# Performance work log

Measured on AMD Instinct MI355X. Metric: run time of the kernel, lower is better.

The kernel has to match this reference:

```python
import jax, jax.numpy as jnp
import numpy as np

B, L = 8, 512
EMB, NHEAD, HD = 512, 8, 64
FFN, NL = 2048, 6
VOCAB, NRE, RING_START, PAD, MAXLEN = 45, 20, 24, 0, 512
NOUT0 = VOCAB - NRE  # 25
NEG = -jnp.inf


def _ln(x, g, b, eps=1e-5):
    m = jnp.mean(x, -1, keepdims=True)
    v = jnp.mean((x - m) ** 2, -1, keepdims=True)
    return (x - m) * jax.lax.rsqrt(v + eps) * g + b


def setup_inputs():
    key = jax.random.key(0)
    ks = jax.random.split(key, 24)
    p = lambda k, shape: jax.random.normal(k, shape, jnp.float32) * 0.02
    return {
        "sequences": jax.random.randint(ks[0], (B, L), 1, VOCAB),  # avoid PAD=0
        "count_sequences": jax.random.randint(ks[1], (B, L), 0, MAXLEN),
        "graph_mask_sequences": jax.random.bernoulli(ks[2], 0.05, (B, L, VOCAB)),
        "valence_mask_sequences": jax.random.bernoulli(ks[3], 0.05, (B, L, VOCAB)),
        "linear_loc_squares": jax.random.randint(ks[4], (B, L, L), 0, MAXLEN + 1),
        "up_loc_squares": jax.random.randint(ks[5], (B, L, L), 0, MAXLEN + 1),
        "down_loc_squares": jax.random.randint(ks[6], (B, L, L), 0, MAXLEN + 1),
        "tok_emb": p(ks[7], (VOCAB, EMB)),
        "cnt_emb": p(ks[8], (MAXLEN, EMB)),
        "lin_loc_emb": p(ks[9], (MAXLEN + 1, NHEAD)),
        "up_loc_emb": p(ks[10], (MAXLEN + 1, NHEAD)),
        "down_loc_emb": p(ks[11], (MAXLEN + 1, NHEAD)),
        "in_proj_w": p(ks[12], (NL, 3 * EMB, EMB)),
        "in_proj_b": jnp.zeros((NL, 3 * EMB), jnp.float32),
        "out_w": p(ks[13], (NL, EMB, EMB)),
        "out_b": jnp.zeros((NL, EMB), jnp.float32),
        "ln1_g": jnp.ones((NL, EMB), jnp.float32),
        "ln1_b": jnp.zeros((NL, EMB), jnp.float32),
        "ln2_g": jnp.ones((NL, EMB), jnp.float32),
        "ln2_b": jnp.zeros((NL, EMB), jnp.float32),
        "ffn_w1": p(ks[14], (NL, FFN, EMB)),
        "ffn_b1": jnp.zeros((NL, FFN), jnp.float32),
        "ffn_w2": p(ks[15], (NL, EMB, FFN)),
        "ffn_b2": jnp.zeros((NL, EMB), jnp.float32),
        "fin_g": jnp.ones((EMB,), jnp.float32),
        "fin_b": jnp.zeros((EMB,), jnp.float32),
        "gen_w": p(ks[16], (NOUT0, EMB)),
        "gen_b": jnp.zeros((NOUT0,), jnp.float32),
        "ring_w0": p(ks[17], (EMB, EMB)),
        "ring_b0": jnp.zeros((EMB,), jnp.float32),
        "ring_w1": p(ks[18], (EMB, EMB)),
        "ring_b1": jnp.zeros((EMB,), jnp.float32),
    }


def _forward(tok_emb, cnt_emb, lin_loc_emb, up_loc_emb, down_loc_emb,
             in_proj_w, in_proj_b, out_w, out_b, ln1_g, ln1_b, ln2_g, ln2_b,
             ffn_w1, ffn_b1, ffn_w2, ffn_b2, fin_g, fin_b, gen_w, gen_b,
             ring_w0, ring_b0, ring_w1, ring_b1,
             sequences, count_sequences, graph_mask_sequences,
             valence_mask_sequences, linear_loc_squares, up_loc_squares,
             down_loc_squares):
    scale_e = jnp.sqrt(jnp.float32(EMB))
    x = tok_emb[sequences] * scale_e + cnt_emb[count_sequences] * scale_e  # (B,L,E)

    # per-head additive attention bias from three (B,L,L) index lookups
    bias = lin_loc_emb[linear_loc_squares] + up_loc_emb[up_loc_squares] + down_loc_emb[down_loc_squares]  # (B,L,L,H)
    bias = jnp.transpose(bias, (0, 3, 1, 2))  # (B,H,Lq,Lk)
    causal = jnp.tril(jnp.ones((L, L), bool))
    attn_bias = jnp.where(causal[None, None], bias, NEG)
    pad = sequences == PAD  # key padding
    attn_bias = jnp.where(pad[:, None, None, :], NEG, attn_bias)

    inv_sqrt_hd = 1.0 / jnp.sqrt(jnp.float32(HD))
    for i in range(NL):  # post-norm TransformerEncoderLayer, gelu
        qkv = jnp.einsum('ble,fe->blf', x, in_proj_w[i]) + in_proj_b[i]
        q, k, v = jnp.split(qkv, 3, axis=-1)
        q = q.reshape(B, L, NHEAD, HD)
        k = k.reshape(B, L, NHEAD, HD)
        v = v.reshape(B, L, NHEAD, HD)
        scores = jnp.einsum('bqhd,bkhd->bhqk', q, k) * inv_sqrt_hd + attn_bias
        a = jax.nn.softmax(scores, axis=-1)
        ctx = jnp.einsum('bhqk,bkhd->bqhd', a, v).reshape(B, L, EMB)
        attn_out = jnp.einsum('ble,fe->blf', ctx, out_w[i]) + out_b[i]
        x = _ln(x + attn_out, ln1_g[i], ln1_b[i])
        h = jax.nn.gelu(jnp.einsum('ble,fe->blf', x, ffn_w1[i]) + ffn_b1[i], approximate=False)
        ff = jnp.einsum('blf,ef->ble', h, ffn_w2[i]) + ffn_b2[i]
        x = _ln(x + ff, ln2_g[i], ln2_b[i])
    x = _ln(x, fin_g, fin_b)

    logits0 = jnp.einsum('ble,oe->blo', x, gen_w) + gen_b  # (B,L,NOUT0)

    # EdgeLogitLayer: scatter ring-start projections into NRE slots
    out0 = jnp.einsum('ble,he->blh', x, ring_w0) + ring_b0
    out1_ = jnp.einsum('ble,he->blh', x, ring_w1) + ring_b1
    ring_start = sequences == RING_START
    idx = jnp.where(ring_start, jnp.cumsum(ring_start.astype(jnp.int32), axis=1), 0)  # (B,L)
    bidx = jnp.arange(B)[:, None]
    slots = jnp.zeros((B, NRE + 1, EMB), x.dtype).at[bidx, idx].set(out1_, mode='drop')
    ring_tab = slots[:, 1:]  # drop slot 0 (non-ring-start writes)
    logits1 = jnp.einsum('ble,bre->blr', out0, ring_tab) * (EMB ** -0.5)

    logits = jnp.concatenate([logits0, logits1], axis=2)  # (B,L,VOCAB)
    logits = jnp.where(graph_mask_sequences, NEG, logits)
    logits = jnp.where(valence_mask_sequences, NEG, logits)
    return logits


def reference(sequences, count_sequences, graph_mask_sequences, valence_mask_sequences,
              linear_loc_squares, up_loc_squares, down_loc_squares,
              tok_emb, cnt_emb, lin_loc_emb, up_loc_emb, down_loc_emb,
              in_proj_w, in_proj_b, out_w, out_b, ln1_g, ln1_b, ln2_g, ln2_b,
              ffn_w1, ffn_b1, ffn_w2, ffn_b2, fin_g, fin_b, gen_w, gen_b,
              ring_w0, ring_b0, ring_w1, ring_b1):
    return _forward(tok_emb, cnt_emb, lin_loc_emb, up_loc_emb, down_loc_emb,
                    in_proj_w, in_proj_b, out_w, out_b, ln1_g, ln1_b, ln2_g, ln2_b,
                    ffn_w1, ffn_b1, ffn_w2, ffn_b2, fin_g, fin_b, gen_w, gen_b,
                    ring_w0, ring_b0, ring_w1, ring_b1,
                    sequences, count_sequences, graph_mask_sequences,
                    valence_mask_sequences, linear_loc_squares, up_loc_squares,
                    down_loc_squares)
```

## Files before the change

### kernel.cpp

```cpp
#include <hip/hip_runtime.h>
#include <cmath>

#define BB 8
#define LL 512
#define EMB 512
#define NHEAD 8
#define HD 64
#define FFN 2048
#define NL 6
#define VOCAB 45
#define NRE 20
#define RING_START 24
#define NOUT0 25
#define BL 4096

#define BIG_NEG -1.0e30f

typedef __bf16 bf16x8 __attribute__((ext_vector_type(8)));
typedef __bf16 bf16x4 __attribute__((ext_vector_type(4)));
typedef float f32x4 __attribute__((ext_vector_type(4)));

__device__ __forceinline__ void ld_g2l(const __bf16* g, __bf16* l) {
  __builtin_amdgcn_global_load_lds(
      (const __attribute__((address_space(1))) unsigned int*)g,
      (__attribute__((address_space(3))) unsigned int*)l, 16, 0, 0);
}

__device__ __forceinline__ int xcd_swizzle_lin() {
  const int nwg = gridDim.x * gridDim.y * gridDim.z;
  int lin = blockIdx.x + gridDim.x * (blockIdx.y + gridDim.y * blockIdx.z);
  if ((nwg & 7) == 0) lin = (lin & 7) * (nwg >> 3) + (lin >> 3);
  return lin;
}

__device__ __forceinline__ float gelu_fast(float v) {
  const float u = v * 0.70710678118654752f;
  const float a = fabsf(u);
  const float t = 1.0f / fmaf(0.3275911f, a, 1.0f);
  float p = fmaf(1.061405429f, t, -1.453152027f);
  p = fmaf(p, t, 1.421413741f);
  p = fmaf(p, t, -0.284496736f);
  p = fmaf(p, t, 0.254829592f);
  p *= t;
  const float er = 1.0f - p * __expf(-a * a);
  const float ers = (u < 0.f) ? -er : er;
  return 0.5f * v * (1.0f + ers);
}

__global__ __launch_bounds__(256) void megacast_kernel(
    const float* __restrict__ s0, const float* __restrict__ s1,
    const float* __restrict__ s2, const float* __restrict__ s3,
    const float* __restrict__ s4, const float* __restrict__ s5,
    const float* __restrict__ s6, const float* __restrict__ s7,
    const float* __restrict__ s8, __bf16* __restrict__ dw,
    __bf16* __restrict__ dt) {
  const int gid = blockIdx.x * 256 + threadIdx.x;
  const int szs[9] = {589824, 196608, 786432, 786432, 32768,
                      32768,  513,    513,    513};
  const float* srcs[9] = {s0, s1, s2, s3, s4, s5, s6, s7, s8};
  int seg = 0, base = 0;
  while (seg < 9 && gid >= base + szs[seg]) { base += szs[seg]; seg++; }
  if (seg >= 9) return;
  const int local = gid - base;
  const float* src = srcs[seg];
  const float4 a = ((const float4*)src)[local * 2];
  const float4 b = ((const float4*)src)[local * 2 + 1];
  bf16x8 v;
  v[0] = (__bf16)a.x; v[1] = (__bf16)a.y; v[2] = (__bf16)a.z; v[3] = (__bf16)a.w;
  v[4] = (__bf16)b.x; v[5] = (__bf16)b.y; v[6] = (__bf16)b.z; v[7] = (__bf16)b.w;
  __bf16* dst = (seg < 6) ? (dw + (size_t)base * 8 + (size_t)local * 8)
                          : (dt + (size_t)(seg - 6) * 4104 + (size_t)local * 8);
  *(bf16x8*)dst = v;
}

__global__ __launch_bounds__(128) void embed_kernel(
    const int* __restrict__ seq, const int* __restrict__ cnt,
    const float* __restrict__ tok_emb, const float* __restrict__ cnt_emb,
    float* __restrict__ x, __bf16* __restrict__ xb) {
  const int row = blockIdx.x;
  const int t = seq[row];
  const int c = cnt[row];
  const float scale = 22.627416997969522f;
  const int j = threadIdx.x * 4;
  float4 tv = *(const float4*)(tok_emb + (size_t)t * EMB + j);
  float4 cv = *(const float4*)(cnt_emb + (size_t)c * EMB + j);
  float4 o;
  o.x = (tv.x + cv.x) * scale;
  o.y = (tv.y + cv.y) * scale;
  o.z = (tv.z + cv.z) * scale;
  o.w = (tv.w + cv.w) * scale;
  *(float4*)(x + (size_t)row * EMB + j) = o;
  bf16x4 h;
  h[0] = (__bf16)o.x; h[1] = (__bf16)o.y; h[2] = (__bf16)o.z; h[3] = (__bf16)o.w;
  *(bf16x4*)(xb + (size_t)row * EMB + j) = h;
}

__global__ __launch_bounds__(256) void bias_kernel(
    const int* __restrict__ lin_sq, const int* __restrict__ up_sq,
    const int* __restrict__ down_sq,
    const __bf16* __restrict__ tl16, const __bf16* __restrict__ tu16,
    const __bf16* __restrict__ td16,
    const int* __restrict__ seq, __bf16* __restrict__ bias) {
  __shared__ __bf16 Tl[513 * 8], Tu[513 * 8], Td[513 * 8];
  __shared__ int seqs[LL];
  const int tid = threadIdx.x;
  const int b = blockIdx.x >> 6;
  const int q0 = (blockIdx.x & 63) * 8;
  for (int i = tid; i < 513; i += 256) {
    *(bf16x8*)&Tl[i * 8] = *(const bf16x8*)&tl16[i * 8];
    *(bf16x8*)&Tu[i * 8] = *(const bf16x8*)&tu16[i * 8];
    *(bf16x8*)&Td[i * 8] = *(const bf16x8*)&td16[i * 8];
  }
  for (int i = tid; i < LL; i += 256) seqs[i] = seq[b * LL + i];
  __syncthreads();
  for (int q = q0; q < q0 + 8; q++) {
    const size_t rbase = ((size_t)(b * LL + q)) * LL;
    for (int k = tid; k <= q; k += 256) {
      const int li = lin_sq[rbase + k], ui = up_sq[rbase + k],
                di = down_sq[rbase + k];
      const bool valid = (seqs[k] != 0);
      bf16x8 a = *(const bf16x8*)&Tl[li * 8];
      bf16x8 u = *(const bf16x8*)&Tu[ui * 8];
      bf16x8 d = *(const bf16x8*)&Td[di * 8];
#pragma unroll
      for (int h = 0; h < NHEAD; h++) {
        float v = valid ? ((float)a[h] + (float)u[h] + (float)d[h])
                        : -INFINITY;
        bias[(((size_t)(b * NHEAD + h) * LL) + q) * LL + k] = (__bf16)v;
      }
    }
  }
}

template <int BM, int BN, int ACT, int OUTBF, int RES, int B2, int SPLITK>
__global__ __launch_bounds__(256) void gemm_mfma_kernel(
    const __bf16* __restrict__ A, const __bf16* __restrict__ W,
    const float* __restrict__ bias, const float* __restrict__ bias2,
    float* __restrict__ C, __bf16* __restrict__ Cb,
    const float* __restrict__ Res, int N, int K, int lda) {
  constexpr int MI = BM / 32;
  constexpr int NI = BN / 32;
  constexpr int LV = (BM == 128 ? 4 : 2) + (BN == 128 ? 4 : 2);
  __shared__ __bf16 As[2][BM * 64];
  __shared__ __bf16 Ws[2][BN * 64];
  const int tid = threadIdx.x;
  const int lane = tid & 63, wave = tid >> 6;
  const int wm = wave >> 1, wn = wave & 1;
  const int q = lane >> 4, l15 = lane & 15;

  const int lin = xcd_swizzle_lin();
  const int bx = lin % gridDim.x;
  const int by = (lin / gridDim.x) % gridDim.y;
  const int kz = SPLITK ? (lin / (gridDim.x * gridDim.y)) : 0;
  const int m0 = by * BM, n0 = bx * BN;

  const int sr = tid >> 3;
  const int sc = (tid & 7) ^ (sr & 7);
  const __bf16* Ag = A + (size_t)(m0 + sr) * lda + sc * 8 + (size_t)kz * K;
  const __bf16* Wg = W + (size_t)(n0 + sr) * lda + sc * 8 + (size_t)kz * K;

  auto stage = [&](int buf, int k0) {
    __bf16* Al = &As[buf][tid * 8];
    __bf16* Wl = &Ws[buf][tid * 8];
    ld_g2l(Ag + k0, Al);
    ld_g2l(Ag + k0 + (size_t)32 * lda, Al + 2048);
    if constexpr (BM == 128) {
      ld_g2l(Ag + k0 + (size_t)64 * lda, Al + 4096);
      ld_g2l(Ag + k0 + (size_t)96 * lda, Al + 6144);
    }
    ld_g2l(Wg + k0, Wl);
    ld_g2l(Wg + k0 + (size_t)32 * lda, Wl + 2048);
    if constexpr (BN == 128) {
      ld_g2l(Wg + k0 + (size_t)64 * lda, Wl + 4096);
      ld_g2l(Wg + k0 + (size_t)96 * lda, Wl + 6144);
    }
  };

  f32x4 acc[MI][NI] = {};

  stage(0, 0);
  int cur = 0;
  for (int k0 = 0; k0 < K; k0 += 64) {
    if (k0 + 64 < K) {
      stage(cur ^ 1, k0 + 64);
      if constexpr (LV == 4)
        asm volatile("s_waitcnt vmcnt(4)" ::: "memory");
      else if constexpr (LV == 6)
        asm volatile("s_waitcnt vmcnt(6)" ::: "memory");
      else
        asm volatile("s_waitcnt vmcnt(8)" ::: "memory");
    } else {
      asm volatile("s_waitcnt vmcnt(0)" ::: "memory");
    }
    __builtin_amdgcn_s_barrier();
    __builtin_amdgcn_sched_barrier(0);
#pragma unroll
    for (int kh = 0; kh < 2; kh++) {
      bf16x8 af[MI], bfr[NI];
      const int ch = ((kh * 4 + q) ^ (l15 & 7)) * 8;
#pragma unroll
      for (int mi = 0; mi < MI; mi++)
        af[mi] = *(const bf16x8*)&As[cur]
                     [(wm * (BM / 2) + mi * 16 + l15) * 64 + ch];
#pragma unroll
      for (int ni = 0; ni < NI; ni++)
        bfr[ni] = *(const bf16x8*)&Ws[cur]
                      [(wn * (BN / 2) + ni * 16 + l15) * 64 + ch];
#pragma unroll
      for (int mi = 0; mi < MI; mi++)
#pragma unroll
        for (int ni = 0; ni < NI; ni++)
          acc[mi][ni] = __builtin_amdgcn_mfma_f32_16x16x32_bf16(
              af[mi], bfr[ni], acc[mi][ni], 0, 0, 0);
    }
    __builtin_amdgcn_sched_barrier(0);
    __builtin_amdgcn_s_barrier();
    cur ^= 1;
  }

  float* Cz = SPLITK ? (C + (size_t)kz * ((size_t)BL * N)) : C;
#pragma unroll
  for (int ni = 0; ni < NI; ni++) {
    const int n = n0 + wn * (BN / 2) + ni * 16 + l15;
    float bv = 0.f;
    if (!SPLITK || kz == 0)
      bv = (B2 && n >= EMB) ? bias2[n - EMB] : bias[n];
#pragma unroll
    for (int mi = 0; mi < MI; mi++) {
#pragma unroll
      for (int r = 0; r < 4; r++) {
        const int m = m0 + wm * (BM / 2) + mi * 16 + q * 4 + r;
        float v = acc[mi][ni][r] + bv;
        if (RES && (!SPLITK || kz == 0)) v += Res[(size_t)m * N + n];
        if (ACT == 1) v = gelu_fast(v);
        if (OUTBF)
          Cb[(size_t)m * N + n] = (__bf16)v;
        else
          Cz[(size_t)m * N + n] = v;
      }
    }
  }
}

__global__ __launch_bounds__(256) void attn_tile2_kernel(
    const __bf16* __restrict__ qkv, const __bf16* __restrict__ bias,
    __bf16* __restrict__ Po, float2* __restrict__ Pml,
    __bf16* __restrict__ ctx) {
  __shared__ __bf16 Ks[64][72];
  __shared__ __bf16 Vt[64][72];
  __shared__ __bf16 Ps[64][72];
  const int tid = threadIdx.x;
  const int lane = tid & 63, w = tid >> 6;
  const int q = lane >> 4, l15 = lane & 15;
  const int lin = xcd_swizzle_lin();
  const int pidx = lin % gridDim.x;
  const int bh = lin / gridDim.x;
  const int b = bh >> 3, h = bh & 7;
  int qt = 0, acc0 = 0;
  while (acc0 + (qt / 2 + 1) <= pidx) { acc0 += qt / 2 + 1; qt++; }
  const int j = pidx - acc0;
  const int q0 = qt * 64;
  const int slot = (bh * 8 + qt) * 4 + j;
  const bool direct = (qt <= 1);
  const float inv_sqrt_hd = 0.125f;

  const int srow = tid >> 2, c0 = (tid & 3) * 16;
  {
    const __bf16* qsrc =
        qkv + (size_t)(b * LL + q0 + srow) * 1536 + h * HD + c0;
    *(bf16x8*)&Ps[srow][c0] = *(const bf16x8*)qsrc;
    *(bf16x8*)&Ps[srow][c0 + 8] = *(const bf16x8*)(qsrc + 8);
  }
  __syncthreads();
  const bf16x8 aq0 = *(const bf16x8*)&Ps[w * 16 + l15][q * 8];
  const bf16x8 aq1 = *(const bf16x8*)&Ps[w * 16 + l15][32 + q * 8];

  f32x4 o4[4] = {};
  float m[4], l[4];
#pragma unroll
  for (int r = 0; r < 4; r++) { m[r] = -INFINITY; l[r] = 0.f; }

  const int ktEnd = (2 * j + 1 <= qt) ? (2 * j + 1) : qt;
  for (int kt = 2 * j; kt <= ktEnd; kt++) {
    const int k0 = kt * 64;
    __syncthreads();
    {
      const __bf16* src = qkv + (size_t)(b * LL + k0 + srow) * 1536 + h * HD;
      bf16x8 kv0 = *(const bf16x8*)(src + 512 + c0);
      bf16x8 kv1 = *(const bf16x8*)(src + 512 + c0 + 8);
      bf16x8 vv0 = *(const bf16x8*)(src + 1024 + c0);
      bf16x8 vv1 = *(const bf16x8*)(src + 1024 + c0 + 8);
      const __bf16* bsrc =
          bias + ((size_t)bh * LL + (q0 + srow)) * LL + k0 + c0;
      bf16x8 bb0 = *(const bf16x8*)bsrc;
      bf16x8 bb1 = *(const bf16x8*)(bsrc + 8);
      *(bf16x8*)&Ks[srow][c0] = kv0;
      *(bf16x8*)&Ks[srow][c0 + 8] = kv1;
      *(bf16x8*)&Ps[srow][c0] = bb0;
      *(bf16x8*)&Ps[srow][c0 + 8] = bb1;
#pragma unroll
      for (int jj = 0; jj < 8; jj++) {
        Vt[c0 + jj][srow] = vv0[jj];
        Vt[c0 + 8 + jj][srow] = vv1[jj];
      }
    }
    __syncthreads();

    f32x4 s4[4] = {};
    __builtin_amdgcn_s_setprio(1);
#pragma unroll
    for (int ni = 0; ni < 4; ni++) {
      bf16x8 bk0 = *(const bf16x8*)&Ks[ni * 16 + l15][q * 8];
      bf16x8 bk1 = *(const bf16x8*)&Ks[ni * 16 + l15][32 + q * 8];
      s4[ni] =
          __builtin_amdgcn_mfma_f32_16x16x32_bf16(aq0, bk0, s4[ni], 0, 0, 0);
      s4[ni] =
          __builtin_amdgcn_mfma_f32_16x16x32_bf16(aq1, bk1, s4[ni], 0, 0, 0);
    }
    __builtin_amdgcn_s_setprio(0);

    const bool diag = (kt == qt);
#pragma unroll
    for (int r = 0; r < 4; r++) {
      const int qrow = w * 16 + q * 4 + r;
      float sv[4];
#pragma unroll
      for (int ni = 0; ni < 4; ni++) {
        sv[ni] = s4[ni][r] * inv_sqrt_hd +
                 (float)Ps[qrow][ni * 16 + l15];
        if (diag && (ni * 16 + l15 > qrow)) sv[ni] = -INFINITY;
      }
      float tm = fmaxf(fmaxf(sv[0], sv[1]), fmaxf(sv[2], sv[3]));
#pragma unroll
      for (int off = 1; off < 16; off <<= 1)
        tm = fmaxf(tm, __shfl_xor(tm, off, 16));
      const float mnew = fmaxf(m[r], tm);
      const float alpha = expf(m[r] - mnew);
      float rs = 0.f;
#pragma unroll
      for (int ni = 0; ni < 4; ni++) {
        const float p = expf(sv[ni] - mnew);
        Ps[qrow][ni * 16 + l15] = (__bf16)p;
        rs += p;
      }
#pragma unroll
      for (int off = 1; off < 16; off <<= 1) rs += __shfl_xor(rs, off, 16);
      l[r] = l[r] * alpha + rs;
      m[r] = mnew;
#pragma unroll
      for (int ni = 0; ni < 4; ni++) o4[ni][r] *= alpha;
    }
    __syncthreads();

    {
      bf16x8 ap0 = *(const bf16x8*)&Ps[w * 16 + l15][q * 8];
      bf16x8 ap1 = *(const bf16x8*)&Ps[w * 16 + l15][32 + q * 8];
      __builtin_amdgcn_s_setprio(1);
#pragma unroll
      for (int ni = 0; ni < 4; ni++) {
        bf16x8 bv0 = *(const bf16x8*)&Vt[ni * 16 + l15][q * 8];
        bf16x8 bv1 = *(const bf16x8*)&Vt[ni * 16 + l15][32 + q * 8];
        o4[ni] =
            __builtin_amdgcn_mfma_f32_16x16x32_bf16(ap0, bv0, o4[ni], 0, 0, 0);
        o4[ni] =
            __builtin_amdgcn_mfma_f32_16x16x32_bf16(ap1, bv1, o4[ni], 0, 0, 0);
      }
      __builtin_amdgcn_s_setprio(0);
    }
  }

  if (direct) {
#pragma unroll
    for (int r = 0; r < 4; r++) {
      const int qrow = w * 16 + q * 4 + r;
      const float inv = 1.0f / l[r];
      __bf16* dst = ctx + (size_t)(b * LL + q0 + qrow) * EMB + h * HD + l15;
#pragma unroll
      for (int ni = 0; ni < 4; ni++) dst[ni * 16] = (__bf16)(o4[ni][r] * inv);
    }
  } else {
#pragma unroll
    for (int r = 0; r < 4; r++) {
      const int qrow = w * 16 + q * 4 + r;
      if (l15 == 0)
        Pml[(size_t)slot * 64 + qrow] = make_float2(m[r], l[r]);
      __bf16* dst = Po + (size_t)slot * 4096 + qrow * 64 + l15;
#pragma unroll
      for (int ni = 0; ni < 4; ni++) dst[ni * 16] = (__bf16)o4[ni][r];
    }
  }
}

__global__ __launch_bounds__(256) void attn_combine_kernel(
    const __bf16* __restrict__ Po, const float2* __restrict__ Pml,
    __bf16* __restrict__ ctx) {
  const int tid = threadIdx.x;
  const int bh = blockIdx.x / 6;
  const int qt = (blockIdx.x % 6) + 2;
  const int b = bh >> 3, h = bh & 7;
  const int nsl = qt / 2 + 1;
  const int slot0 = (bh * 8 + qt) * 4;
  __shared__ float wls[4][64];
  __shared__ float invl[64];
  if (tid < 64) {
    float mg = -3.0e38f;
    for (int s = 0; s < nsl; s++)
      mg = fmaxf(mg, Pml[(size_t)(slot0 + s) * 64 + tid].x);
    float lsum = 0.f;
    for (int s = 0; s < nsl; s++) {
      const float2 ml = Pml[(size_t)(slot0 + s) * 64 + tid];
      const float wk = expf(ml.x - mg);
      wls[s][tid] = wk;
      lsum += ml.y * wk;
    }
    invl[tid] = 1.0f / lsum;
  }
  __syncthreads();
  const int row = tid >> 2, d0 = (tid & 3) * 16;
  float acc[16] = {};
  for (int s = 0; s < nsl; s++) {
    const __bf16* src = Po + (size_t)(slot0 + s) * 4096 + row * 64 + d0;
    const float wk = wls[s][row];
    bf16x8 v0 = *(const bf16x8*)src;
    bf16x8 v1 = *(const bf16x8*)(src + 8);
#pragma unroll
    for (int jj = 0; jj < 8; jj++) {
      acc[jj] += (float)v0[jj] * wk;
      acc[8 + jj] += (float)v1[jj] * wk;
    }
  }
  const float il = invl[row];
  bf16x8 o0, o1;
#pragma unroll
  for (int jj = 0; jj < 8; jj++) {
    o0[jj] = (__bf16)(acc[jj] * il);
    o1[jj] = (__bf16)(acc[8 + jj] * il);
  }
  __bf16* dst = ctx + (size_t)(b * LL + qt * 64 + row) * EMB + h * HD + d0;
  *(bf16x8*)dst = o0;
  *(bf16x8*)(dst + 8) = o1;
}

template <int NSUM>
__global__ __launch_bounds__(256) void add_ln_kernel(
    const float* __restrict__ xin, const float* __restrict__ g,
    const float* __restrict__ bta, float* __restrict__ out,
    __bf16* __restrict__ outb) {
  const int row = blockIdx.x;
  const int tid = threadIdx.x;
  float v0 = 0.f, v1 = 0.f;
#pragma unroll
  for (int sId = 0; sId < NSUM; sId++) {
    const float* xr = xin + (size_t)sId * BL * EMB + (size_t)row * EMB;
    v0 += xr[tid * 2];
    v1 += xr[tid * 2 + 1];
  }
  float s = v0 + v1, ss = v0 * v0 + v1 * v1;
#pragma unroll
  for (int off = 1; off < 64; off <<= 1) {
    s += __shfl_xor(s, off, 64);
    ss += __shfl_xor(ss, off, 64);
  }
  __shared__ float sbuf[8];
  const int wave = tid >> 6, lane = tid & 63;
  if (lane == 0) { sbuf[wave] = s; sbuf[4 + wave] = ss; }
  __syncthreads();
  s = sbuf[0] + sbuf[1] + sbuf[2] + sbuf[3];
  ss = sbuf[4] + sbuf[5] + sbuf[6] + sbuf[7];
  const float mean = s * (1.0f / EMB);
  const float var = ss * (1.0f / EMB) - mean * mean;
  const float rstd = rsqrtf(var + 1e-5f);
  const float o0 = (v0 - mean) * rstd * g[tid * 2] + bta[tid * 2];
  const float o1 = (v1 - mean) * rstd * g[tid * 2 + 1] + bta[tid * 2 + 1];
  float* orow = out + (size_t)row * EMB;
  orow[tid * 2] = o0;
  orow[tid * 2 + 1] = o1;
  if (outb) {
    __bf16* brow = outb + (size_t)row * EMB;
    brow[tid * 2] = (__bf16)o0;
    brow[tid * 2 + 1] = (__bf16)o1;
  }
}

__global__ __launch_bounds__(512) void ring_scatter_kernel(
    const int* __restrict__ seq, const float* __restrict__ o01,
    float* __restrict__ ring_tab) {
  const int b = blockIdx.x;
  const int tid = threadIdx.x;
  float* rt = ring_tab + (size_t)b * NRE * EMB;
  __shared__ int pos[NRE];
  __shared__ int wcnt[8];
  __shared__ int total;
  const bool flag = (seq[b * LL + tid] == RING_START);
  const unsigned long long msk = __ballot(flag);
  const int wave = tid >> 6, lane = tid & 63;
  if (lane == 0) wcnt[wave] = __popcll(msk);
  for (int i = tid; i < NRE * EMB; i += 512) rt[i] = 0.f;
  __syncthreads();
  if (flag) {
    int base = 0;
    for (int w2 = 0; w2 < wave; w2++) base += wcnt[w2];
    const int ord = base + __popcll(msk & ((1ull << lane) - 1ull));
    if (ord < NRE) pos[ord] = tid;
  }
  if (tid == 0) {
    int t = 0;
    for (int w2 = 0; w2 < 8; w2++) t += wcnt[w2];
    total = (t < NRE) ? t : NRE;
  }
  __syncthreads();
  const int n = total;
  for (int r = 0; r < n; r++) {
    const float* src = o01 + (size_t)(b * LL + pos[r]) * 1024 + 512;
    rt[r * EMB + tid] = src[tid];
  }
}

__global__ __launch_bounds__(256) void head_kernel(
    const float* __restrict__ xf, const float* __restrict__ o01,
    const float* __restrict__ ring_tab, const float* __restrict__ gen_w,
    const float* __restrict__ gen_b, const int* __restrict__ gmask,
    const int* __restrict__ vmask, float* __restrict__ out) {
  const int row = blockIdx.x;
  const int b = row >> 9;
  const int tid = threadIdx.x;
  __shared__ float xr[EMB], o0s[EMB];
  {
    float2 a = ((const float2*)(xf + (size_t)row * EMB))[tid];
    ((float2*)xr)[tid] = a;
    float2 c = ((const float2*)(o01 + (size_t)row * 1024))[tid];
    ((float2*)o0s)[tid] = c;
  }
  __syncthreads();
  const int wave = tid >> 6, lane = tid & 63;
  for (int o = wave; o < VOCAB; o += 4) {
    const float* wrow;
    const float* src;
    float bv, scale;
    if (o < NOUT0) {
      wrow = gen_w + (size_t)o * EMB;
      bv = gen_b[o];
      src = xr;
      scale = 1.0f;
    } else {
      wrow = ring_tab + ((size_t)b * NRE + (o - NOUT0)) * EMB;
      bv = 0.0f;
      src = o0s;
      scale = 0.044194173824159216f;
    }
    float sum = 0.f;
#pragma unroll
    for (int j = 0; j < 8; j++) {
      const int d = lane + 64 * j;
      sum += src[d] * wrow[d];
    }
#pragma unroll
    for (int off = 1; off < 64; off <<= 1) sum += __shfl_xor(sum, off, 64);
    if (lane == 0) {
      float v = sum * scale + bv;
      const size_t oidx = (size_t)row * VOCAB + o;
      if (gmask[oidx] != 0 || vmask[oidx] != 0) v = BIG_NEG;
      out[oidx] = v;
    }
  }
}

extern "C" void kernel_launch(void* const* d_in, const int* in_sizes, int n_in,
                              void* d_out, int out_size, void* d_ws,
                              size_t ws_size, hipStream_t stream) {
  const int* seq = (const int*)d_in[0];
  const int* cnt = (const int*)d_in[1];
  const int* gmask = (const int*)d_in[2];
  const int* vmask = (const int*)d_in[3];
  const int* lin_sq = (const int*)d_in[4];
  const int* up_sq = (const int*)d_in[5];
  const int* down_sq = (const int*)d_in[6];
  const float* tok_emb = (const float*)d_in[7];
  const float* cnt_emb = (const float*)d_in[8];
  const float* lin_e = (const float*)d_in[9];
  const float* up_e = (const float*)d_in[10];
  const float* down_e = (const float*)d_in[11];
  const float* in_proj_w = (const float*)d_in[12];
  const float* in_proj_b = (const float*)d_in[13];
  const float* out_w = (const float*)d_in[14];
  const float* out_b = (const float*)d_in[15];
  const float* ln1_g = (const float*)d_in[16];
  const float* ln1_b = (const float*)d_in[17];
  const float* ln2_g = (const float*)d_in[18];
  const float* ln2_b = (const float*)d_in[19];
  const float* ffn_w1 = (const float*)d_in[20];
  const float* ffn_b1 = (const float*)d_in[21];
  const float* ffn_w2 = (const float*)d_in[22];
  const float* ffn_b2 = (const float*)d_in[23];
  const float* fin_g = (const float*)d_in[24];
  const float* fin_b = (const float*)d_in[25];
  const float* gen_w = (const float*)d_in[26];
  const float* gen_b = (const float*)d_in[27];
  const float* ring_w0 = (const float*)d_in[28];
  const float* ring_b0 = (const float*)d_in[29];
  const float* ring_w1 = (const float*)d_in[30];
  const float* ring_b1 = (const float*)d_in[31];

  char* p = (char*)d_ws;
  auto alloc_f = [&](size_t n) { float* r = (float*)p; p += n * 4; return r; };
  auto alloc_h = [&](size_t n) { __bf16* r = (__bf16*)p; p += n * 2; return r; };

  float* x = alloc_f((size_t)BL * EMB);
  float* pbuf = alloc_f((size_t)2 * BL * EMB);
  float* xfb = alloc_f((size_t)BL * EMB);
  float* o01b = alloc_f((size_t)BL * 1024);
  float* ringb = alloc_f((size_t)BB * NRE * EMB);
  float2* attn_pml = (float2*)alloc_f((size_t)2048 * 64 * 2);
  __bf16* attn_po = alloc_h((size_t)2048 * 4096);
  __bf16* biasb = alloc_h((size_t)BB * NHEAD * LL * LL);
  __bf16* xb = alloc_h((size_t)BL * EMB);
  __bf16* qkvb16 = alloc_h((size_t)BL * 3 * EMB);
  __bf16* ctxb = alloc_h((size_t)BL * EMB);
  __bf16* hb = alloc_h((size_t)BL * FFN);
  __bf16* xfb16 = alloc_h((size_t)BL * EMB);
  __bf16* wqkv = alloc_h((size_t)NL * 3 * EMB * EMB);
  __bf16* wout = alloc_h((size_t)NL * EMB * EMB);
  __bf16* wf1 = alloc_h((size_t)NL * FFN * EMB);
  __bf16* wf2 = alloc_h((size_t)NL * EMB * FFN);
  __bf16* wr01 = alloc_h((size_t)2 * EMB * EMB);
  __bf16* tl16 = hb;
  __bf16* tu16 = hb + 4104;
  __bf16* td16 = hb + 8208;

  megacast_kernel<<<9478, 256, 0, stream>>>(
      in_proj_w, out_w, ffn_w1, ffn_w2, ring_w0, ring_w1, lin_e, up_e, down_e,
      wqkv, tl16);

  embed_kernel<<<BL, 128, 0, stream>>>(seq, cnt, tok_emb, cnt_emb, x, xb);
  bias_kernel<<<BB * 64, 256, 0, stream>>>(lin_sq, up_sq, down_sq, tl16, tu16,
                                           td16, seq, biasb);

  for (int i = 0; i < NL; i++) {
    gemm_mfma_kernel<64, 128, 0, 1, 0, 0, 0>
        <<<dim3(12, 64), 256, 0, stream>>>(
        xb, wqkv + (size_t)i * 3 * EMB * EMB, in_proj_b + (size_t)i * 3 * EMB,
        nullptr, nullptr, qkvb16, nullptr, 3 * EMB, EMB, EMB);
    attn_tile2_kernel<<<dim3(20, 64), 256, 0, stream>>>(qkvb16, biasb, attn_po,
                                                        attn_pml, ctxb);
    attn_combine_kernel<<<384, 256, 0, stream>>>(attn_po, attn_pml, ctxb);
    gemm_mfma_kernel<64, 64, 0, 0, 1, 0, 0><<<dim3(8, 64), 256, 0, stream>>>(
        ctxb, wout + (size_t)i * EMB * EMB, out_b + (size_t)i * EMB, nullptr,
        pbuf, nullptr, x, EMB, EMB, EMB);
    add_ln_kernel<1><<<BL, 256, 0, stream>>>(
        pbuf, ln1_g + (size_t)i * EMB, ln1_b + (size_t)i * EMB, x, xb);
    gemm_mfma_kernel<128, 128, 1, 1, 0, 0, 0>
        <<<dim3(16, 32), 256, 0, stream>>>(
        xb, wf1 + (size_t)i * FFN * EMB, ffn_b1 + (size_t)i * FFN, nullptr,
        nullptr, hb, nullptr, FFN, EMB, EMB);
    gemm_mfma_kernel<64, 64, 0, 0, 1, 0, 1>
        <<<dim3(8, 64, 2), 256, 0, stream>>>(
        hb, wf2 + (size_t)i * EMB * FFN, ffn_b2 + (size_t)i * EMB, nullptr,
        pbuf, nullptr, x, EMB, FFN / 2, FFN);
    add_ln_kernel<2><<<BL, 256, 0, stream>>>(
        pbuf, ln2_g + (size_t)i * EMB, ln2_b + (size_t)i * EMB, x, xb);
  }

  add_ln_kernel<1><<<BL, 256, 0, stream>>>(x, fin_g, fin_b, xfb, xfb16);
  gemm_mfma_kernel<64, 128, 0, 0, 0, 1, 0><<<dim3(8, 64), 256, 0, stream>>>(
      xfb16, wr01, ring_b0, ring_b1, o01b, nullptr, nullptr, 1024, EMB, EMB);
  ring_scatter_kernel<<<BB, 512, 0, stream>>>(seq, o01b, ringb);
  head_kernel<<<BL, 256, 0, stream>>>(xfb, o01b, ringb, gen_w, gen_b, gmask,
                                      vmask, (float*)d_out);
}
```

Baseline: 880.7 us.

## Fuse attention split-KV combine into tile kernel via last-block atomic counter

Removes the separate attention combine kernel. Each split-KV block of a query tile writes its partial output and increments an atomic counter, and the last block to arrive merges the partials and writes the context. Counters are zeroed inside the existing megacast kernel, which gets one extra block, and each layer uses its own counter slice. This saves one kernel launch per layer and the extra pass over the partials, at the cost of threadfences, an atomic, and serialized combine work in the last-arriving block.

```diff
diff --git a/kernel.cpp b/kernel.cpp
--- a/kernel.cpp
+++ b/kernel.cpp
@@ -53,8 +53,9 @@
     const float* __restrict__ s4, const float* __restrict__ s5,
     const float* __restrict__ s6, const float* __restrict__ s7,
     const float* __restrict__ s8, __bf16* __restrict__ dw,
-    __bf16* __restrict__ dt) {
+    __bf16* __restrict__ dt, int* __restrict__ acnt) {
   const int gid = blockIdx.x * 256 + threadIdx.x;
+  if (gid < NL * 512) acnt[gid] = 0;
   const int szs[9] = {589824, 196608, 786432, 786432, 32768,
                       32768,  513,    513,    513};
   const float* srcs[9] = {s0, s1, s2, s3, s4, s5, s6, s7, s8};
@@ -245,10 +246,11 @@
 __global__ __launch_bounds__(256) void attn_tile2_kernel(
     const __bf16* __restrict__ qkv, const __bf16* __restrict__ bias,
     __bf16* __restrict__ Po, float2* __restrict__ Pml,
-    __bf16* __restrict__ ctx) {
+    __bf16* __restrict__ ctx, int* __restrict__ acnt) {
   __shared__ __bf16 Ks[64][72];
   __shared__ __bf16 Vt[64][72];
   __shared__ __bf16 Ps[64][72];
+  __shared__ int lastFlag;
   const int tid = threadIdx.x;
   const int lane = tid & 63, w = tid >> 6;
   const int q = lane >> 4, l15 = lane & 15;
@@ -260,7 +262,9 @@
   while (acc0 + (qt / 2 + 1) <= pidx) { acc0 += qt / 2 + 1; qt++; }
   const int j = pidx - acc0;
   const int q0 = qt * 64;
-  const int slot = (bh * 8 + qt) * 4 + j;
+  const int nsl = qt / 2 + 1;
+  const int slot0 = (bh * 8 + qt) * 4;
+  const int slot = slot0 + j;
   const bool direct = (qt <= 1);
   const float inv_sqrt_hd = 0.125f;
 
@@ -378,30 +382,30 @@
 #pragma unroll
       for (int ni = 0; ni < 4; ni++) dst[ni * 16] = (__bf16)(o4[ni][r] * inv);
     }
-  } else {
-#pragma unroll
-    for (int r = 0; r < 4; r++) {
-      const int qrow = w * 16 + q * 4 + r;
-      if (l15 == 0)
-        Pml[(size_t)slot * 64 + qrow] = make_float2(m[r], l[r]);
-      __bf16* dst = Po + (size_t)slot * 4096 + qrow * 64 + l15;
-#pragma unroll
-      for (int ni = 0; ni < 4; ni++) dst[ni * 16] = (__bf16)o4[ni][r];
-    }
-  }
-}
-
-__global__ __launch_bounds__(256) void attn_combine_kernel(
-    const __bf16* __restrict__ Po, const float2* __restrict__ Pml,
-    __bf16* __restrict__ ctx) {
-  const int tid = threadIdx.x;
-  const int bh = blockIdx.x / 6;
-  const int qt = (blockIdx.x % 6) + 2;
-  const int b = bh >> 3, h = bh & 7;
-  const int nsl = qt / 2 + 1;
-  const int slot0 = (bh * 8 + qt) * 4;
-  __shared__ float wls[4][64];
-  __shared__ float invl[64];
+    return;
+  }
+
+#pragma unroll
+  for (int r = 0; r < 4; r++) {
+    const int qrow = w * 16 + q * 4 + r;
+    if (l15 == 0)
+      Pml[(size_t)slot * 64 + qrow] = make_float2(m[r], l[r]);
+    __bf16* dst = Po + (size_t)slot * 4096 + qrow * 64 + l15;
+#pragma unroll
+    for (int ni = 0; ni < 4; ni++) dst[ni * 16] = (__bf16)o4[ni][r];
+  }
+  __threadfence();
+  __syncthreads();
+  if (tid == 0) {
+    const int old = atomicAdd(&acnt[bh * 8 + qt], 1);
+    lastFlag = (old == nsl - 1);
+  }
+  __syncthreads();
+  if (!lastFlag) return;
+  __threadfence();
+
+  float* wls = (float*)&Ks[0][0];
+  float* invl = (float*)&Vt[0][0];
   if (tid < 64) {
     float mg = -3.0e38f;
     for (int s = 0; s < nsl; s++)
@@ -410,7 +414,7 @@
     for (int s = 0; s < nsl; s++) {
       const float2 ml = Pml[(size_t)(slot0 + s) * 64 + tid];
       const float wk = expf(ml.x - mg);
-      wls[s][tid] = wk;
+      wls[s * 64 + tid] = wk;
       lsum += ml.y * wk;
     }
     invl[tid] = 1.0f / lsum;
@@ -420,7 +424,7 @@
   float acc[16] = {};
   for (int s = 0; s < nsl; s++) {
     const __bf16* src = Po + (size_t)(slot0 + s) * 4096 + row * 64 + d0;
-    const float wk = wls[s][row];
+    const float wk = wls[s * 64 + row];
     bf16x8 v0 = *(const bf16x8*)src;
     bf16x8 v1 = *(const bf16x8*)(src + 8);
 #pragma unroll
@@ -436,7 +440,7 @@
     o0[jj] = (__bf16)(acc[jj] * il);
     o1[jj] = (__bf16)(acc[8 + jj] * il);
   }
-  __bf16* dst = ctx + (size_t)(b * LL + qt * 64 + row) * EMB + h * HD + d0;
+  __bf16* dst = ctx + (size_t)(b * LL + q0 + row) * EMB + h * HD + d0;
   *(bf16x8*)dst = o0;
   *(bf16x8*)(dst + 8) = o1;
 }
@@ -610,6 +614,7 @@
   float* xfb = alloc_f((size_t)BL * EMB);
   float* o01b = alloc_f((size_t)BL * 1024);
   float* ringb = alloc_f((size_t)BB * NRE * EMB);
+  int* acnt = (int*)alloc_f((size_t)NL * 512);
   float2* attn_pml = (float2*)alloc_f((size_t)2048 * 64 * 2);
   __bf16* attn_po = alloc_h((size_t)2048 * 4096);
   __bf16* biasb = alloc_h((size_t)BB * NHEAD * LL * LL);
@@ -627,9 +632,9 @@
   __bf16* tu16 = hb + 4104;
   __bf16* td16 = hb + 8208;
 
-  megacast_kernel<<<9478, 256, 0, stream>>>(
+  megacast_kernel<<<9479, 256, 0, stream>>>(
       in_proj_w, out_w, ffn_w1, ffn_w2, ring_w0, ring_w1, lin_e, up_e, down_e,
-      wqkv, tl16);
+      wqkv, tl16, acnt);
 
   embed_kernel<<<BL, 128, 0, stream>>>(seq, cnt, tok_emb, cnt_emb, x, xb);
   bias_kernel<<<BB * 64, 256, 0, stream>>>(lin_sq, up_sq, down_sq, tl16, tu16,
@@ -640,9 +645,8 @@
         <<<dim3(12, 64), 256, 0, stream>>>(
         xb, wqkv + (size_t)i * 3 * EMB * EMB, in_proj_b + (size_t)i * 3 * EMB,
         nullptr, nullptr, qkvb16, nullptr, 3 * EMB, EMB, EMB);
-    attn_tile2_kernel<<<dim3(20, 64), 256, 0, stream>>>(qkvb16, biasb, attn_po,
-                                                        attn_pml, ctxb);
-    attn_combine_kernel<<<384, 256, 0, stream>>>(attn_po, attn_pml, ctxb);
+    attn_tile2_kernel<<<dim3(20, 64), 256, 0, stream>>>(
+        qkvb16, biasb, attn_po, attn_pml, ctxb, acnt + (size_t)i * 512);
     gemm_mfma_kernel<64, 64, 0, 0, 1, 0, 0><<<dim3(8, 64), 256, 0, stream>>>(
         ctxb, wout + (size_t)i * EMB * EMB, out_b + (size_t)i * EMB, nullptr,
         pbuf, nullptr, x, EMB, EMB, EMB);
```

Result: slower. 1.987 ms (+125.7%).
